# Kernel optimization log

Measured on AMD Instinct MI355X. Metric: run time of the kernel, lower is better.

The kernel has to match this reference:

```python
import jax, jax.numpy as jnp
import numpy as np

CLASS_NUM = 8
OUT_SIZE = 160
EPS = 1e-8


def conv1x1(x, w, b):
    # x: [B,Cin,H,W], w: [Cout,Cin], b: [Cout]
    return jnp.einsum('oc,bchw->bohw', w, x) + b[None, :, None, None]


def setup_inputs() -> dict:
    key = jax.random.key(0)
    ks = jax.random.split(key, 8)
    Cin, Cout = 256, 128
    B, H, W = 16, 80, 80
    feature = jax.random.normal(ks[0], (B, Cin, H, W), dtype=jnp.float32)
    fusion_label = jax.random.randint(ks[1], (B, 1, OUT_SIZE, OUT_SIZE), 0, CLASS_NUM, dtype=jnp.int64) if jax.config.jax_enable_x64 else jax.random.randint(ks[1], (B, 1, OUT_SIZE, OUT_SIZE), 0, CLASS_NUM).astype(jnp.int32)
    w1 = jax.random.normal(ks[2], (2 * Cin, Cin), dtype=jnp.float32) * 0.05
    b1 = jnp.zeros((2 * Cin,), dtype=jnp.float32)
    w2 = jax.random.normal(ks[3], (Cin, 2 * Cin), dtype=jnp.float32) * 0.05
    b2 = jnp.zeros((Cin,), dtype=jnp.float32)
    w3 = jax.random.normal(ks[4], (Cout, Cin), dtype=jnp.float32) * 0.05
    b3 = jnp.zeros((Cout,), dtype=jnp.float32)
    return {"feature": feature, "fusion_label": fusion_label,
            "w1": w1, "b1": b1, "w2": w2, "b2": b2, "w3": w3, "b3": b3}


def reference(feature, fusion_label, w1, b1, w2, b2, w3, b3):
    # 1x1 conv stack with ReLUs (conv1 in the torch module)
    f = jax.nn.relu(conv1x1(feature, w1, b1))
    f = jax.nn.relu(conv1x1(f, w2, b2))
    f2 = jax.nn.relu(conv1x1(f, w3, b3))
    B, C = f2.shape[0], f2.shape[1]
    # bilinear resize, half-pixel centers == torch align_corners=False
    f3 = jax.image.resize(f2, (B, C, OUT_SIZE, OUT_SIZE), method='bilinear', antialias=False)
    # per-class masked mean pooling (segment mean over spatial positions)
    lbl = fusion_label[:, 0]  # [B,H,W]
    onehot = jax.nn.one_hot(lbl, CLASS_NUM, dtype=f3.dtype)  # [B,H,W,K]
    counts = onehot.sum((1, 2))  # [B,K]
    pooled = jnp.einsum('bhwk,bchw->bkc', onehot, f3) / (counts + EPS)[..., None]
    presence = (counts > 0).astype(jnp.int32)  # which (image, class) rows the torch code would emit
    return pooled, presence
```

## Files before the change

kernel.cpp:

```cpp
#include <hip/hip_runtime.h>

#define B_SZ   16
#define P_IN   6400
#define H_IN   80
#define OUTHW  160
#define NCLASS 8

typedef __attribute__((ext_vector_type(8))) short  short8v;
typedef __attribute__((ext_vector_type(4))) float  f32x4;
typedef __attribute__((ext_vector_type(4))) unsigned short ushort4v;
typedef __attribute__((ext_vector_type(2))) unsigned short ushort2v;

__device__ __forceinline__ unsigned short f2bf(float x) {
    union { float f; unsigned int u; } v; v.f = x;
    unsigned int r = v.u + 0x7fffu + ((v.u >> 16) & 1u);
    return (unsigned short)(r >> 16);
}
__device__ __forceinline__ float bf2f(unsigned short h) {
    union { unsigned int u; float f; } v; v.u = ((unsigned int)h) << 16;
    return v.f;
}

__device__ __forceinline__ void gload16(const unsigned short* g, unsigned short* lds) {
    __builtin_amdgcn_global_load_lds(
        (const __attribute__((address_space(1))) unsigned int*)g,
        (__attribute__((address_space(3))) unsigned int*)lds, 16, 0, 0);
}

__global__ void wprep(const float* __restrict__ w, unsigned short* __restrict__ wh,
                      unsigned short* __restrict__ wl, int n) {
    int i = blockIdx.x * 256 + threadIdx.x;
    if (i < n) {
        float v = w[i];
        unsigned short h = f2bf(v);
        wh[i] = h;
        wl[i] = f2bf(v - bf2f(h));
    }
}

__global__ void fprep(const float* __restrict__ feat, unsigned short* __restrict__ xh) {
    __shared__ float t[32][257];
    const int b = blockIdx.y, p0 = blockIdx.x * 32;
    const int pi = threadIdx.x & 31, cg = threadIdx.x >> 5;
    const float* fb = feat + (size_t)b * 256 * P_IN;
#pragma unroll 4
    for (int cc = 0; cc < 32; ++cc) {
        int c = cc * 8 + cg;
        t[pi][c] = fb[(size_t)c * P_IN + p0 + pi];
    }
    __syncthreads();
    const int rr  = threadIdx.x >> 7;
    const int cc2 = threadIdx.x & 127;
#pragma unroll 4
    for (int r = 0; r < 32; r += 2) {
        const int row = r + rr;
        ushort2v u;
        u.x = f2bf(t[row][cc2 * 2]);
        u.y = f2bf(t[row][cc2 * 2 + 1]);
        *(ushort2v*)&xh[((size_t)b * P_IN + p0 + row) * 256 + cc2 * 2] = u;
    }
}

template<int K, int NM>
__global__ __launch_bounds__(256, 3)
void conv_mfma(const unsigned short* __restrict__ Wh, const unsigned short* __restrict__ Wl,
               const float* __restrict__ bias,
               const unsigned short* __restrict__ X, unsigned short* __restrict__ Y)
{
    constexpr int M = NM * 128;
    __shared__ unsigned short As_h[8192], As_l[8192], Bs[8192];
    const int tid = threadIdx.x, lane = tid & 63, w = tid >> 6;
    const int wm = w >> 1, wn = w & 1;

    const int nb = gridDim.x;
    const int id = blockIdx.x;
    const int wg = (id & 7) * (nb >> 3) + (id >> 3);
    const int b   = wg / (50 * NM);
    const int rem = wg - b * (50 * NM);
    const int n0 = (rem / NM) * 128;
    const int m0 = (rem - (rem / NM) * NM) * 128;

    const size_t xbase = ((size_t)b * P_IN + n0) * K;

    f32x4 acc[4][4];
#pragma unroll
    for (int i = 0; i < 4; ++i)
#pragma unroll
        for (int j = 0; j < 4; ++j) acc[i][j] = (f32x4)0.f;

    const int srow = lane >> 3;
    const int scol = lane & 7;

    for (int k0 = 0; k0 < K; k0 += 64) {
#pragma unroll
        for (int q = 0; q < 4; ++q) {
            const int c   = w * 4 + q;
            const int row = c * 8 + srow;
            const int kc  = scol ^ (row & 7);
            const size_t ga = (size_t)(m0 + row) * K + k0 + kc * 8;
            const size_t gx = xbase + (size_t)row * K + k0 + kc * 8;
            const int lo = c * 512;
            gload16(Wh + ga, &As_h[lo]);
            gload16(Wl + ga, &As_l[lo]);
            gload16(X + gx, &Bs[lo]);
        }
        __syncthreads();
#pragma unroll
        for (int s = 0; s < 2; ++s) {
            short8v ah[4], al[4], bb[4];
            const int kc = s * 4 + (lane >> 4);
#pragma unroll
            for (int mi = 0; mi < 4; ++mi) {
                const int m = wm * 64 + mi * 16 + (lane & 15);
                const int off = m * 64 + ((kc ^ (m & 7)) << 3);
                ah[mi] = *(const short8v*)&As_h[off];
                al[mi] = *(const short8v*)&As_l[off];
            }
#pragma unroll
            for (int ni = 0; ni < 4; ++ni) {
                const int n = wn * 64 + ni * 16 + (lane & 15);
                const int off = n * 64 + ((kc ^ (n & 7)) << 3);
                bb[ni] = *(const short8v*)&Bs[off];
            }
#pragma unroll
            for (int mi = 0; mi < 4; ++mi)
#pragma unroll
                for (int ni = 0; ni < 4; ++ni) {
                    acc[mi][ni] = __builtin_amdgcn_mfma_f32_16x16x32_bf16(ah[mi], bb[ni], acc[mi][ni], 0, 0, 0);
                    acc[mi][ni] = __builtin_amdgcn_mfma_f32_16x16x32_bf16(al[mi], bb[ni], acc[mi][ni], 0, 0, 0);
                }
        }
        __syncthreads();
    }

    const int lhi = lane >> 4;
#pragma unroll
    for (int mi = 0; mi < 4; ++mi) {
        const int m_base = m0 + wm * 64 + mi * 16 + lhi * 4;
        const float4 b4 = *(const float4*)&bias[m_base];
#pragma unroll
        for (int ni = 0; ni < 4; ++ni) {
            const int n = n0 + wn * 64 + ni * 16 + (lane & 15);
            const size_t o = ((size_t)b * P_IN + n) * M + m_base;
            ushort4v u;
            u.x = f2bf(fmaxf(acc[mi][ni][0] + b4.x, 0.f));
            u.y = f2bf(fmaxf(acc[mi][ni][1] + b4.y, 0.f));
            u.z = f2bf(fmaxf(acc[mi][ni][2] + b4.z, 0.f));
            u.w = f2bf(fmaxf(acc[mi][ni][3] + b4.w, 0.f));
            *(ushort4v*)&Y[o] = u;
        }
    }
}

__global__ void label_scatter(const int* __restrict__ lbl,
                              float* __restrict__ g, float* __restrict__ counts)
{
    __shared__ float hist[NCLASS];
    const int b   = blockIdx.x;
    const int tid = threadIdx.x;
    const int pix = blockIdx.y * 256 + tid;
    if (tid < NCLASS) hist[tid] = 0.f;
    __syncthreads();

    const int i = pix / OUTHW;
    const int j = pix - i * OUTHW;
    const int k = lbl[(size_t)b * (OUTHW * OUTHW) + pix];

    const int mi = i >> 1, mj = j >> 1;
    int y0, y1, x0, x1; float wy0, wy1, wx0, wx1;
    if (i & 1) { y0 = mi; y1 = (mi < H_IN - 1) ? mi + 1 : H_IN - 1; wy0 = 0.75f; wy1 = 0.25f; }
    else       { y0 = (mi > 0) ? mi - 1 : 0; y1 = mi;               wy0 = 0.25f; wy1 = 0.75f; }
    if (j & 1) { x0 = mj; x1 = (mj < H_IN - 1) ? mj + 1 : H_IN - 1; wx0 = 0.75f; wx1 = 0.25f; }
    else       { x0 = (mj > 0) ? mj - 1 : 0; x1 = mj;               wx0 = 0.25f; wx1 = 0.75f; }

    float* gb = g + ((size_t)(b * NCLASS + k)) * P_IN;
    atomicAdd(&gb[y0 * H_IN + x0], wy0 * wx0);
    atomicAdd(&gb[y0 * H_IN + x1], wy0 * wx1);
    atomicAdd(&gb[y1 * H_IN + x0], wy1 * wx0);
    atomicAdd(&gb[y1 * H_IN + x1], wy1 * wx1);

    atomicAdd(&hist[k], 1.f);
    __syncthreads();
    if (tid < NCLASS) atomicAdd(&counts[b * NCLASS + tid], hist[tid]);
}

__global__ __launch_bounds__(256)
void pool2(const unsigned short* __restrict__ f3, const float* __restrict__ g,
           float* __restrict__ pooled)
{
    __shared__ float sg[NCLASS][800];
    const int b = blockIdx.x, chunk = blockIdx.y;
    const int tid = threadIdx.x;
#pragma unroll
    for (int i = 0; i < 25; ++i) {
        int idx = i * 256 + tid;
        int k = idx / 800, p = idx - k * 800;
        sg[k][p] = g[((size_t)b * NCLASS + k) * P_IN + chunk * 800 + p];
    }
    __syncthreads();

    const int c  = tid & 127;
    const int kg = tid >> 7;
    float acc0 = 0.f, acc1 = 0.f, acc2 = 0.f, acc3 = 0.f;
    const unsigned short* fb = f3 + ((size_t)b * P_IN + chunk * 800) * 128 + c;
    for (int p = 0; p < 800; ++p) {
        const float fv = bf2f(fb[(size_t)p * 128]);
        acc0 = fmaf(fv, sg[kg * 4 + 0][p], acc0);
        acc1 = fmaf(fv, sg[kg * 4 + 1][p], acc1);
        acc2 = fmaf(fv, sg[kg * 4 + 2][p], acc2);
        acc3 = fmaf(fv, sg[kg * 4 + 3][p], acc3);
    }
    atomicAdd(&pooled[((size_t)b * NCLASS + kg * 4 + 0) * 128 + c], acc0);
    atomicAdd(&pooled[((size_t)b * NCLASS + kg * 4 + 1) * 128 + c], acc1);
    atomicAdd(&pooled[((size_t)b * NCLASS + kg * 4 + 2) * 128 + c], acc2);
    atomicAdd(&pooled[((size_t)b * NCLASS + kg * 4 + 3) * 128 + c], acc3);
}

__global__ void finalize(const float* __restrict__ pooled, const float* __restrict__ counts,
                         float* __restrict__ out)
{
    const int b = blockIdx.x;
#pragma unroll
    for (int i = threadIdx.x; i < NCLASS * 128; i += 256) {
        const int k = i >> 7;
        const float cnt = counts[b * NCLASS + k];
        out[(size_t)b * NCLASS * 128 + i] = pooled[(size_t)b * NCLASS * 128 + i] / (cnt + 1e-8f);
    }
    if (threadIdx.x < NCLASS)
        out[B_SZ * NCLASS * 128 + b * NCLASS + threadIdx.x] =
            (counts[b * NCLASS + threadIdx.x] > 0.f) ? 1.f : 0.f;
}

extern "C" void kernel_launch(void* const* d_in, const int* in_sizes, int n_in,
                              void* d_out, int out_size, void* d_ws, size_t ws_size,
                              hipStream_t stream)
{
    const float* feature = (const float*)d_in[0];
    const int*   lbl     = (const int*)d_in[1];
    const float* w1 = (const float*)d_in[2];
    const float* b1 = (const float*)d_in[3];
    const float* w2 = (const float*)d_in[4];
    const float* b2 = (const float*)d_in[5];
    const float* w3 = (const float*)d_in[6];
    const float* b3 = (const float*)d_in[7];
    float* out = (float*)d_out;

    char* ws = (char*)d_ws;
    unsigned short* Xh  = (unsigned short*)(ws);
    unsigned short* f1  = (unsigned short*)(ws + 52428800);
    unsigned short* f2  = (unsigned short*)(ws + 157286400);
    unsigned short* f3  = (unsigned short*)(ws + 209715200);
    unsigned short* Wh1 = (unsigned short*)(ws + 235929600);
    unsigned short* Wl1 = (unsigned short*)(ws + 236191744);
    unsigned short* Wh2 = (unsigned short*)(ws + 236453888);
    unsigned short* Wl2 = (unsigned short*)(ws + 236716032);
    unsigned short* Wh3 = (unsigned short*)(ws + 236978176);
    unsigned short* Wl3 = (unsigned short*)(ws + 237043712);
    float* g      = (float*)(ws + 237109248);
    float* counts = (float*)(ws + 240386048);
    float* pooled = (float*)(ws + 240386560);

    hipMemsetAsync(g, 0, 3276800 + 512 + 65536, stream);

    wprep<<<512, 256, 0, stream>>>(w1, Wh1, Wl1, 512 * 256);
    wprep<<<512, 256, 0, stream>>>(w2, Wh2, Wl2, 256 * 512);
    wprep<<<128, 256, 0, stream>>>(w3, Wh3, Wl3, 128 * 256);
    fprep<<<dim3(200, 16), 256, 0, stream>>>(feature, Xh);

    conv_mfma<256, 4><<<3200, 256, 0, stream>>>(Wh1, Wl1, b1, Xh, f1);
    conv_mfma<512, 2><<<1600, 256, 0, stream>>>(Wh2, Wl2, b2, f1, f2);
    conv_mfma<256, 1><<<800,  256, 0, stream>>>(Wh3, Wl3, b3, f2, f3);

    label_scatter<<<dim3(B_SZ, (OUTHW * OUTHW) / 256), 256, 0, stream>>>(lbl, g, counts);
    pool2<<<dim3(B_SZ, 8), 256, 0, stream>>>(f3, g, pooled);
    finalize<<<B_SZ, 256, 0, stream>>>(pooled, counts, out);
}
```

Measured before the change: 406.8 us.

## Double-buffer conv GEMM LDS tiles, merge weight prep, and slab-local label scatter

The 1x1-conv MFMA kernel now uses a K-step of 32 with two LDS buffers, so global-to-LDS loads for the next step are issued while MFMAs run on the current one, and one barrier per step replaces two. The LDS swizzle is changed to suit the narrower tile. The three weight-splitting launches are merged into one kernel. The label scatter now accumulates into per-slab shared-memory grids and writes each slab once, removing global float atomics and the large memset of g. In exchange the conv loop runs twice as many iterations with less work each, and the scatter reads halo label rows redundantly.

Result: faster. 396.6 us (-2.5%).

```diff
diff --git a/kernel.cpp b/kernel.cpp
--- a/kernel.cpp
+++ b/kernel.cpp
@@ -27,15 +27,22 @@
         (__attribute__((address_space(3))) unsigned int*)lds, 16, 0, 0);
 }
 
-__global__ void wprep(const float* __restrict__ w, unsigned short* __restrict__ wh,
-                      unsigned short* __restrict__ wl, int n) {
+__global__ void wprep3(const float* __restrict__ w1, const float* __restrict__ w2,
+                       const float* __restrict__ w3,
+                       unsigned short* __restrict__ h1, unsigned short* __restrict__ l1,
+                       unsigned short* __restrict__ h2, unsigned short* __restrict__ l2,
+                       unsigned short* __restrict__ h3, unsigned short* __restrict__ l3)
+{
     int i = blockIdx.x * 256 + threadIdx.x;
-    if (i < n) {
-        float v = w[i];
-        unsigned short h = f2bf(v);
-        wh[i] = h;
-        wl[i] = f2bf(v - bf2f(h));
-    }
+    const float* src; unsigned short *h, *l; int off;
+    if (i < 131072)      { src = w1; h = h1; l = l1; off = i; }
+    else if (i < 262144) { src = w2; h = h2; l = l2; off = i - 131072; }
+    else                 { src = w3; h = h3; l = l3; off = i - 262144;
+                           if (off >= 32768) return; }
+    float v = src[off];
+    unsigned short hi = f2bf(v);
+    h[off] = hi;
+    l[off] = f2bf(v - bf2f(hi));
 }
 
 __global__ void fprep(const float* __restrict__ feat, unsigned short* __restrict__ xh) {
@@ -67,20 +74,22 @@
                const float* __restrict__ bias,
                const unsigned short* __restrict__ X, unsigned short* __restrict__ Y)
 {
-    constexpr int M = NM * 128;
-    __shared__ unsigned short As_h[8192], As_l[8192], Bs[8192];
+    constexpr int M  = NM * 128;
+    constexpr int NK = K / 32;
+    __shared__ unsigned short As_h[2][4096], As_l[2][4096], Bs[2][4096];
     const int tid = threadIdx.x, lane = tid & 63, w = tid >> 6;
     const int wm = w >> 1, wn = w & 1;
 
     const int nb = gridDim.x;
     const int id = blockIdx.x;
     const int wg = (id & 7) * (nb >> 3) + (id >> 3);
-    const int b   = wg / (50 * NM);
-    const int rem = wg - b * (50 * NM);
+    const int bb  = wg / (50 * NM);
+    const int rem = wg - bb * (50 * NM);
     const int n0 = (rem / NM) * 128;
     const int m0 = (rem - (rem / NM) * NM) * 128;
 
-    const size_t xbase = ((size_t)b * P_IN + n0) * K;
+    const size_t abase = (size_t)m0 * K;
+    const size_t xbase = ((size_t)bb * P_IN + n0) * K;
 
     f32x4 acc[4][4];
 #pragma unroll
@@ -88,50 +97,65 @@
 #pragma unroll
         for (int j = 0; j < 4; ++j) acc[i][j] = (f32x4)0.f;
 
-    const int srow = lane >> 3;
-    const int scol = lane & 7;
-
-    for (int k0 = 0; k0 < K; k0 += 64) {
-#pragma unroll
-        for (int q = 0; q < 4; ++q) {
-            const int c   = w * 4 + q;
-            const int row = c * 8 + srow;
-            const int kc  = scol ^ (row & 7);
-            const size_t ga = (size_t)(m0 + row) * K + k0 + kc * 8;
-            const size_t gx = xbase + (size_t)row * K + k0 + kc * 8;
-            const int lo = c * 512;
-            gload16(Wh + ga, &As_h[lo]);
-            gload16(Wl + ga, &As_l[lo]);
-            gload16(X + gx, &Bs[lo]);
+    int s_row[2], s_k8[2], s_lo[2];
+#pragma unroll
+    for (int q = 0; q < 2; ++q) {
+        const int ch = 2 * w + q;
+        s_row[q] = ch * 16 + (lane >> 2);
+        s_k8[q]  = ((((lane & 3) - (s_row[q] >> 1)) & 3) << 3);
+        s_lo[q]  = ch * 512;
+    }
+    int off_a[4], off_b[4];
+    const int gsel = lane >> 4;
+#pragma unroll
+    for (int mi = 0; mi < 4; ++mi) {
+        const int r = wm * 64 + mi * 16 + (lane & 15);
+        off_a[mi] = r * 32 + (((gsel + (r >> 1)) & 3) << 3);
+    }
+#pragma unroll
+    for (int ni = 0; ni < 4; ++ni) {
+        const int r = wn * 64 + ni * 16 + (lane & 15);
+        off_b[ni] = r * 32 + (((gsel + (r >> 1)) & 3) << 3);
+    }
+
+#define STAGE(buf, kt) do {                                                   \
+    _Pragma("unroll")                                                         \
+    for (int q = 0; q < 2; ++q) {                                             \
+        const size_t kof = (size_t)(kt) * 32 + s_k8[q];                       \
+        const size_t gW  = abase + (size_t)s_row[q] * K + kof;                \
+        const size_t gX  = xbase + (size_t)s_row[q] * K + kof;                \
+        gload16(Wh + gW, &As_h[buf][s_lo[q]]);                                \
+        gload16(Wl + gW, &As_l[buf][s_lo[q]]);                                \
+        gload16(X  + gX, &Bs[buf][s_lo[q]]);                                  \
+    }                                                                         \
+} while (0)
+
+    int cur = 0;
+    STAGE(0, 0);
+    __syncthreads();
+
+    for (int t = 0; t < NK; ++t) {
+        if (t + 1 < NK) STAGE(cur ^ 1, t + 1);
+        short8v ah[4], al[4], bv[4];
+#pragma unroll
+        for (int mi = 0; mi < 4; ++mi) {
+            ah[mi] = *(const short8v*)&As_h[cur][off_a[mi]];
+            al[mi] = *(const short8v*)&As_l[cur][off_a[mi]];
         }
+#pragma unroll
+        for (int ni = 0; ni < 4; ++ni)
+            bv[ni] = *(const short8v*)&Bs[cur][off_b[ni]];
+#pragma unroll
+        for (int mi = 0; mi < 4; ++mi)
+#pragma unroll
+            for (int ni = 0; ni < 4; ++ni) {
+                acc[mi][ni] = __builtin_amdgcn_mfma_f32_16x16x32_bf16(ah[mi], bv[ni], acc[mi][ni], 0, 0, 0);
+                acc[mi][ni] = __builtin_amdgcn_mfma_f32_16x16x32_bf16(al[mi], bv[ni], acc[mi][ni], 0, 0, 0);
+            }
         __syncthreads();
-#pragma unroll
-        for (int s = 0; s < 2; ++s) {
-            short8v ah[4], al[4], bb[4];
-            const int kc = s * 4 + (lane >> 4);
-#pragma unroll
-            for (int mi = 0; mi < 4; ++mi) {
-                const int m = wm * 64 + mi * 16 + (lane & 15);
-                const int off = m * 64 + ((kc ^ (m & 7)) << 3);
-                ah[mi] = *(const short8v*)&As_h[off];
-                al[mi] = *(const short8v*)&As_l[off];
-            }
-#pragma unroll
-            for (int ni = 0; ni < 4; ++ni) {
-                const int n = wn * 64 + ni * 16 + (lane & 15);
-                const int off = n * 64 + ((kc ^ (n & 7)) << 3);
-                bb[ni] = *(const short8v*)&Bs[off];
-            }
-#pragma unroll
-            for (int mi = 0; mi < 4; ++mi)
-#pragma unroll
-                for (int ni = 0; ni < 4; ++ni) {
-                    acc[mi][ni] = __builtin_amdgcn_mfma_f32_16x16x32_bf16(ah[mi], bb[ni], acc[mi][ni], 0, 0, 0);
-                    acc[mi][ni] = __builtin_amdgcn_mfma_f32_16x16x32_bf16(al[mi], bb[ni], acc[mi][ni], 0, 0, 0);
-                }
-        }
-        __syncthreads();
-    }
+        cur ^= 1;
+    }
+#undef STAGE
 
     const int lhi = lane >> 4;
 #pragma unroll
@@ -141,7 +165,7 @@
 #pragma unroll
         for (int ni = 0; ni < 4; ++ni) {
             const int n = n0 + wn * 64 + ni * 16 + (lane & 15);
-            const size_t o = ((size_t)b * P_IN + n) * M + m_base;
+            const size_t o = ((size_t)bb * P_IN + n) * M + m_base;
             ushort4v u;
             u.x = f2bf(fmaxf(acc[mi][ni][0] + b4.x, 0.f));
             u.y = f2bf(fmaxf(acc[mi][ni][1] + b4.y, 0.f));
@@ -152,35 +176,47 @@
     }
 }
 
-__global__ void label_scatter(const int* __restrict__ lbl,
-                              float* __restrict__ g, float* __restrict__ counts)
-{
+__global__ __launch_bounds__(256)
+void label_scatter(const int* __restrict__ lbl, float* __restrict__ g,
+                   float* __restrict__ counts)
+{
+    __shared__ float sg[NCLASS][8][80];
     __shared__ float hist[NCLASS];
-    const int b   = blockIdx.x;
+    const int b = blockIdx.x, slab = blockIdx.y;
     const int tid = threadIdx.x;
-    const int pix = blockIdx.y * 256 + tid;
+    const int r0 = slab * 8;
+    for (int i = tid; i < NCLASS * 8 * 80; i += 256) ((float*)sg)[i] = 0.f;
     if (tid < NCLASS) hist[tid] = 0.f;
     __syncthreads();
 
-    const int i = pix / OUTHW;
-    const int j = pix - i * OUTHW;
-    const int k = lbl[(size_t)b * (OUTHW * OUTHW) + pix];
-
-    const int mi = i >> 1, mj = j >> 1;
-    int y0, y1, x0, x1; float wy0, wy1, wx0, wx1;
-    if (i & 1) { y0 = mi; y1 = (mi < H_IN - 1) ? mi + 1 : H_IN - 1; wy0 = 0.75f; wy1 = 0.25f; }
-    else       { y0 = (mi > 0) ? mi - 1 : 0; y1 = mi;               wy0 = 0.25f; wy1 = 0.75f; }
-    if (j & 1) { x0 = mj; x1 = (mj < H_IN - 1) ? mj + 1 : H_IN - 1; wx0 = 0.75f; wx1 = 0.25f; }
-    else       { x0 = (mj > 0) ? mj - 1 : 0; x1 = mj;               wx0 = 0.25f; wx1 = 0.75f; }
-
-    float* gb = g + ((size_t)(b * NCLASS + k)) * P_IN;
-    atomicAdd(&gb[y0 * H_IN + x0], wy0 * wx0);
-    atomicAdd(&gb[y0 * H_IN + x1], wy0 * wx1);
-    atomicAdd(&gb[y1 * H_IN + x0], wy1 * wx0);
-    atomicAdd(&gb[y1 * H_IN + x1], wy1 * wx1);
-
-    atomicAdd(&hist[k], 1.f);
-    __syncthreads();
+    const int ibase = 2 * r0 - 1;
+    for (int idx = tid; idx < 18 * 160; idx += 256) {
+        const int ir = idx / 160, j = idx - ir * 160;
+        const int i = ibase + ir;
+        if (i < 0 || i >= OUTHW) continue;
+        const int k = lbl[(size_t)b * (OUTHW * OUTHW) + i * OUTHW + j];
+        const int mi = i >> 1, mj = j >> 1;
+        int y0, y1, x0, x1; float wy0, wy1, wx0, wx1;
+        if (i & 1) { y0 = mi; y1 = (mi < H_IN - 1) ? mi + 1 : H_IN - 1; wy0 = 0.75f; wy1 = 0.25f; }
+        else       { y0 = (mi > 0) ? mi - 1 : 0; y1 = mi;               wy0 = 0.25f; wy1 = 0.75f; }
+        if (j & 1) { x0 = mj; x1 = (mj < H_IN - 1) ? mj + 1 : H_IN - 1; wx0 = 0.75f; wx1 = 0.25f; }
+        else       { x0 = (mj > 0) ? mj - 1 : 0; x1 = mj;               wx0 = 0.25f; wx1 = 0.75f; }
+        if (mi >= r0 && mi < r0 + 8) atomicAdd(&hist[k], 1.f);
+        const int ry0 = y0 - r0, ry1 = y1 - r0;
+        if (ry0 >= 0 && ry0 < 8) {
+            atomicAdd(&sg[k][ry0][x0], wy0 * wx0);
+            atomicAdd(&sg[k][ry0][x1], wy0 * wx1);
+        }
+        if (ry1 >= 0 && ry1 < 8) {
+            atomicAdd(&sg[k][ry1][x0], wy1 * wx0);
+            atomicAdd(&sg[k][ry1][x1], wy1 * wx1);
+        }
+    }
+    __syncthreads();
+    for (int i = tid; i < NCLASS * 8 * 80; i += 256) {
+        const int k = i / 640, rem2 = i - k * 640;
+        g[((size_t)b * NCLASS + k) * P_IN + r0 * 80 + rem2] = ((const float*)sg)[i];
+    }
     if (tid < NCLASS) atomicAdd(&counts[b * NCLASS + tid], hist[tid]);
 }
 
@@ -260,18 +296,16 @@
     float* counts = (float*)(ws + 240386048);
     float* pooled = (float*)(ws + 240386560);
 
-    hipMemsetAsync(g, 0, 3276800 + 512 + 65536, stream);
-
-    wprep<<<512, 256, 0, stream>>>(w1, Wh1, Wl1, 512 * 256);
-    wprep<<<512, 256, 0, stream>>>(w2, Wh2, Wl2, 256 * 512);
-    wprep<<<128, 256, 0, stream>>>(w3, Wh3, Wl3, 128 * 256);
+    hipMemsetAsync(counts, 0, 512 + 65536, stream);
+
+    wprep3<<<1152, 256, 0, stream>>>(w1, w2, w3, Wh1, Wl1, Wh2, Wl2, Wh3, Wl3);
     fprep<<<dim3(200, 16), 256, 0, stream>>>(feature, Xh);
 
     conv_mfma<256, 4><<<3200, 256, 0, stream>>>(Wh1, Wl1, b1, Xh, f1);
     conv_mfma<512, 2><<<1600, 256, 0, stream>>>(Wh2, Wl2, b2, f1, f2);
     conv_mfma<256, 1><<<800,  256, 0, stream>>>(Wh3, Wl3, b3, f2, f3);
 
-    label_scatter<<<dim3(B_SZ, (OUTHW * OUTHW) / 256), 256, 0, stream>>>(lbl, g, counts);
+    label_scatter<<<dim3(B_SZ, 10), 256, 0, stream>>>(lbl, g, counts);
     pool2<<<dim3(B_SZ, 8), 256, 0, stream>>>(f3, g, pooled);
     finalize<<<B_SZ, 256, 0, stream>>>(pooled, counts, out);
 }
```
